# Performance work log

Measured on AMD Instinct MI355X. Metric: run time of the kernel, lower is better.

## Reference

```python
import jax, jax.numpy as jnp
import numpy as np

HIDDEN = 4096
N_HEADS = 32
N_KV_HEADS = 8
HEAD_SIZE = HIDDEN // N_HEADS  # 128
ROPE_THETA = 10000.0
SEQ_LEN = 1024
BATCH = 4


def setup_inputs() -> dict:
    key = jax.random.key(0)
    k1, k2, k3 = jax.random.split(key, 3)
    scale = 1.0 / np.sqrt(HIDDEN)
    hidden_states = jax.random.normal(k1, (BATCH * SEQ_LEN, HIDDEN), dtype=jnp.float32)
    w_qkv = jax.random.normal(k2, ((N_HEADS + 2 * N_KV_HEADS) * HEAD_SIZE, HIDDEN), dtype=jnp.float32) * scale
    w_o = jax.random.normal(k3, (HIDDEN, N_HEADS * HEAD_SIZE), dtype=jnp.float32) * scale
    return {"hidden_states": hidden_states, "w_qkv": w_qkv, "w_o": w_o, "seq_len": SEQ_LEN}


def _rope(x, pos, theta):
    # x: [B, S, H, D]; pos: [S] absolute positions; rotate-half (LLAMA/NeoX) style
    d = x.shape[-1]
    inv_freq = 1.0 / (theta ** (jnp.arange(0, d, 2, dtype=jnp.float32) / d))  # [D/2]
    ang = pos.astype(jnp.float32)[:, None] * inv_freq[None, :]  # [S, D/2]
    cos = jnp.cos(ang)[None, :, None, :]
    sin = jnp.sin(ang)[None, :, None, :]
    x1, x2 = jnp.split(x, 2, axis=-1)
    return jnp.concatenate([x1 * cos - x2 * sin, x2 * cos + x1 * sin], axis=-1)


def reference(hidden_states, w_qkv, w_o, seq_len):
    total, hidden = hidden_states.shape
    B = total // seq_len
    hd = HEAD_SIZE
    # fused QKV projection (bias-free), split like the torch module
    qkv = hidden_states @ w_qkv.T  # [T, (H+2K)*hd]
    q, k, v = jnp.split(qkv, [N_HEADS * hd, (N_HEADS + N_KV_HEADS) * hd], axis=1)
    q = q.reshape(B, seq_len, N_HEADS, hd)
    k = k.reshape(B, seq_len, N_KV_HEADS, hd)
    v = v.reshape(B, seq_len, N_KV_HEADS, hd)
    # inline RoPE (ROPE_LLAMA) on q and k at absolute positions
    pos = jnp.arange(seq_len)
    q = _rope(q, pos, ROPE_THETA)
    k = _rope(k, pos, ROPE_THETA)
    # GQA: map each q head to its kv head (kv_head_mapping = repeat_interleave)
    groups = N_HEADS // N_KV_HEADS
    k = jnp.repeat(k, groups, axis=2)  # [B, S, H, hd]
    v = jnp.repeat(v, groups, axis=2)
    scale = hd ** -0.5
    scores = jnp.einsum('bqhd,bkhd->bhqk', q, k) * scale  # [B, H, S, S]
    causal = jnp.tril(jnp.ones((seq_len, seq_len), dtype=bool))
    scores = jnp.where(causal[None, None], scores, jnp.finfo(scores.dtype).min)
    probs = jax.nn.softmax(scores, axis=-1)
    attn = jnp.einsum('bhqk,bkhd->bqhd', probs, v).reshape(total, N_HEADS * hd)
    return attn @ w_o.T  # [T, hidden]
```

## Files before the change

### kernel.cpp

```cpp
#include <hip/hip_runtime.h>


typedef short bf16x8 __attribute__((ext_vector_type(8)));
typedef short bf16x4 __attribute__((ext_vector_type(4)));
typedef float floatx4 __attribute__((ext_vector_type(4)));
typedef unsigned short u16x4 __attribute__((ext_vector_type(4)));

__device__ __forceinline__ unsigned short f2bf(float f) {
  unsigned u = __float_as_uint(f);
  u += 0x7FFFu + ((u >> 16) & 1u);
  return (unsigned short)(u >> 16);
}
__device__ __forceinline__ float bf2f(unsigned short h) {
  return __uint_as_float(((unsigned)h) << 16);
}

__device__ __forceinline__ void async16(const void* g, void* l) {
  __builtin_amdgcn_global_load_lds(
      (const __attribute__((address_space(1))) unsigned int*)g,
      (__attribute__((address_space(3))) unsigned int*)l, 16, 0, 0);
}

__global__ void cvt_f32_bf16(const float4* __restrict__ in,
                             u16x4* __restrict__ out, int n4) {
  int i = blockIdx.x * 256 + threadIdx.x;
  if (i < n4) {
    float4 v = in[i];
    u16x4 o;
    o.x = f2bf(v.x); o.y = f2bf(v.y); o.z = f2bf(v.z); o.w = f2bf(v.w);
    out[i] = o;
  }
}

template <int OUT_BF16>
__global__ __launch_bounds__(256) void gemm_bt(
    const unsigned short* __restrict__ A, const unsigned short* __restrict__ B,
    void* __restrict__ Cout, int M, int N, int K) {
  __shared__ __align__(16) unsigned short As[128 * 32];
  __shared__ __align__(16) unsigned short Bs[128 * 32];
  const int tid = threadIdx.x;
  const int wave = tid >> 6, lane = tid & 63;
  const int quad = lane >> 4, l16 = lane & 15;
  const int bm = blockIdx.y << 7, bn = blockIdx.x << 7;
  const int wm = (wave >> 1) << 6;
  const int wn = (wave & 1) << 6;

  floatx4 acc[4][4];
#pragma unroll
  for (int i = 0; i < 4; ++i)
#pragma unroll
    for (int j = 0; j < 4; ++j) acc[i][j] = (floatx4){0.f, 0.f, 0.f, 0.f};

  const int r0 = tid >> 2;
  const int o0 = (tid & 3) << 3;
  const unsigned short* A0 = A + (size_t)(bm + r0) * K + o0;
  const unsigned short* A1 = A0 + (size_t)64 * K;
  const unsigned short* B0 = B + (size_t)(bn + r0) * K + o0;
  const unsigned short* B1 = B0 + (size_t)64 * K;
  char* lA0 = (char*)As + wave * 1024;
  char* lA1 = lA0 + 4096;
  char* lB0 = (char*)Bs + wave * 1024;
  char* lB1 = lB0 + 4096;

  const unsigned short* Asp = As + (wm + l16) * 32 + quad * 8;
  const unsigned short* Bsp = Bs + (wn + l16) * 32 + quad * 8;

  for (int k0 = 0; k0 < K; k0 += 32) {
    __syncthreads();
    async16(A0 + k0, lA0);
    async16(A1 + k0, lA1);
    async16(B0 + k0, lB0);
    async16(B1 + k0, lB1);
    __syncthreads();
    bf16x8 af[4], bfr[4];
#pragma unroll
    for (int mi = 0; mi < 4; ++mi) af[mi] = *(const bf16x8*)(Asp + mi * 512);
#pragma unroll
    for (int ni = 0; ni < 4; ++ni) bfr[ni] = *(const bf16x8*)(Bsp + ni * 512);
#pragma unroll
    for (int mi = 0; mi < 4; ++mi)
#pragma unroll
      for (int ni = 0; ni < 4; ++ni)
        acc[mi][ni] = __builtin_amdgcn_mfma_f32_16x16x32_bf16(
            af[mi], bfr[ni], acc[mi][ni], 0, 0, 0);
  }

  const int row0 = bm + wm + quad * 4;
  const int col0 = bn + wn + l16;
  if (OUT_BF16) {
    unsigned short* C = (unsigned short*)Cout;
#pragma unroll
    for (int mi = 0; mi < 4; ++mi)
#pragma unroll
      for (int ni = 0; ni < 4; ++ni)
#pragma unroll
        for (int r = 0; r < 4; ++r)
          C[(size_t)(row0 + mi * 16 + r) * N + (col0 + ni * 16)] =
              f2bf(acc[mi][ni][r]);
  } else {
    float* C = (float*)Cout;
#pragma unroll
    for (int mi = 0; mi < 4; ++mi)
#pragma unroll
      for (int ni = 0; ni < 4; ++ni)
#pragma unroll
        for (int r = 0; r < 4; ++r)
          C[(size_t)(row0 + mi * 16 + r) * N + (col0 + ni * 16)] =
              acc[mi][ni][r];
  }
}

__global__ void rope_k_kernel(unsigned short* __restrict__ qkv) {
  const int t = blockIdx.x;
  const int s = t & 1023;
  const int head = 32 + blockIdx.y * 4 + (threadIdx.x >> 6);
  const int d = threadIdx.x & 63;
  unsigned short* p = qkv + (size_t)t * 6144 + head * 128;
  float x1 = bf2f(p[d]), x2 = bf2f(p[d + 64]);
  float inv_freq = exp2f((float)d * -0.20762050593046015f);
  float ang = (float)s * inv_freq;
  float c, sn;
  __sincosf(ang, &sn, &c);
  p[d] = f2bf(x1 * c - x2 * sn);
  p[d + 64] = f2bf(x2 * c + x1 * sn);
}

__global__ __launch_bounds__(256, 3) void flash_attn(
    const unsigned short* __restrict__ qkv, unsigned short* __restrict__ aout) {
  const int qt = gridDim.x - 1 - blockIdx.x;
  const int h = blockIdx.y, b = blockIdx.z;
  const int kh = h >> 2;
  const int tid = threadIdx.x;
  const int wave = tid >> 6, lane = tid & 63;
  const int quad = lane >> 4, l16 = lane & 15;
  const int q0 = qt << 6;

  __shared__ __align__(16) unsigned short Ks[64][136];
  __shared__ __align__(16) unsigned short Vt[128][68];
  __shared__ __align__(16) unsigned short Ps[64][68];

  bf16x8 qf[4];
  {
    const int qrow = q0 + wave * 16 + l16;
    const unsigned short* qp =
        qkv + (size_t)((b << 10) + qrow) * 6144 + h * 128 + quad * 8;
#pragma unroll
    for (int ks = 0; ks < 4; ++ks) qf[ks] = *(const bf16x8*)(qp + ks * 32);
    const float pos = (float)qrow;
    const float scale = 0.08838834764831845f;
#pragma unroll
    for (int ks = 0; ks < 2; ++ks)
#pragma unroll
      for (int e = 0; e < 8; ++e) {
        int d = ks * 32 + quad * 8 + e;
        float ang = pos * exp2f((float)d * -0.20762050593046015f);
        float c, sn;
        __sincosf(ang, &sn, &c);
        float x1 = bf2f((unsigned short)qf[ks][e]);
        float x2 = bf2f((unsigned short)qf[ks + 2][e]);
        qf[ks][e] = (short)f2bf((x1 * c - x2 * sn) * scale);
        qf[ks + 2][e] = (short)f2bf((x2 * c + x1 * sn) * scale);
      }
  }

  floatx4 o_acc[8];
#pragma unroll
  for (int i = 0; i < 8; ++i) o_acc[i] = (floatx4){0.f, 0.f, 0.f, 0.f};
  float l_lane[4] = {0.f, 0.f, 0.f, 0.f};

  const int krow = tid >> 4, kcol = (tid & 15) << 3;
  const int vrb = (tid & 15) << 2, vcol = (tid >> 4) << 3;
  const unsigned short* kp =
      qkv + (size_t)(b << 10) * 6144 + 4096 + kh * 128;
  const unsigned short* vp =
      qkv + (size_t)(b << 10) * 6144 + 5120 + kh * 128;

  bf16x8 kreg[4], vreg[4];
#pragma unroll
  for (int j = 0; j < 4; ++j)
    kreg[j] = *(const bf16x8*)(kp + (size_t)(krow + j * 16) * 6144 + kcol);
#pragma unroll
  for (int j = 0; j < 4; ++j)
    vreg[j] = *(const bf16x8*)(vp + (size_t)(vrb + j) * 6144 + vcol);

  for (int t = 0; t <= qt; ++t) {
    __syncthreads();
#pragma unroll
    for (int j = 0; j < 4; ++j)
      *(bf16x8*)&Ks[krow + j * 16][kcol] = kreg[j];
#pragma unroll
    for (int e = 0; e < 8; ++e) {
      bf16x4 w = {vreg[0][e], vreg[1][e], vreg[2][e], vreg[3][e]};
      *(bf16x4*)&Vt[vcol + e][vrb] = w;
    }
    __syncthreads();
    if (t < qt) {
      const size_t nb = (size_t)((t + 1) << 6) * 6144;
#pragma unroll
      for (int j = 0; j < 4; ++j)
        kreg[j] = *(const bf16x8*)(kp + nb + (size_t)(krow + j * 16) * 6144 + kcol);
#pragma unroll
      for (int j = 0; j < 4; ++j)
        vreg[j] = *(const bf16x8*)(vp + nb + (size_t)(vrb + j) * 6144 + vcol);
    }

    floatx4 sacc[4];
#pragma unroll
    for (int ni = 0; ni < 4; ++ni) sacc[ni] = (floatx4){0.f, 0.f, 0.f, 0.f};
#pragma unroll
    for (int ks = 0; ks < 4; ++ks)
#pragma unroll
      for (int ni = 0; ni < 4; ++ni) {
        bf16x8 kf = *(const bf16x8*)&Ks[ni * 16 + l16][ks * 32 + quad * 8];
        sacc[ni] =
            __builtin_amdgcn_mfma_f32_16x16x32_bf16(qf[ks], kf, sacc[ni], 0, 0, 0);
      }

    const bool masked = (t == qt);
#pragma unroll
    for (int r = 0; r < 4; ++r) {
      float rs = 0.f;
#pragma unroll
      for (int ni = 0; ni < 4; ++ni) {
        float e = __expf(sacc[ni][r]);
        if (masked && (ni * 16 + l16) > (wave * 16 + quad * 4 + r)) e = 0.f;
        rs += e;
        Ps[wave * 16 + quad * 4 + r][ni * 16 + l16] = f2bf(e);
      }
      l_lane[r] += rs;
    }
    asm volatile("s_waitcnt lgkmcnt(0)" ::: "memory");

#pragma unroll
    for (int ks2 = 0; ks2 < 2; ++ks2) {
      bf16x8 pf = *(const bf16x8*)&Ps[wave * 16 + l16][ks2 * 32 + quad * 8];
#pragma unroll
      for (int n8 = 0; n8 < 8; ++n8) {
        bf16x8 vf = *(const bf16x8*)&Vt[n8 * 16 + l16][ks2 * 32 + quad * 8];
        o_acc[n8] =
            __builtin_amdgcn_mfma_f32_16x16x32_bf16(pf, vf, o_acc[n8], 0, 0, 0);
      }
    }
  }

#pragma unroll
  for (int r = 0; r < 4; ++r) {
    float l = l_lane[r];
#pragma unroll
    for (int off = 1; off < 16; off <<= 1) l += __shfl_xor(l, off, 64);
    float inv = 1.0f / l;
    int row = q0 + wave * 16 + quad * 4 + r;
    unsigned short* op = aout + (size_t)((b << 10) + row) * 4096 + h * 128;
#pragma unroll
    for (int n8 = 0; n8 < 8; ++n8)
      op[n8 * 16 + l16] = f2bf(o_acc[n8][r] * inv);
  }
}

extern "C" void kernel_launch(void* const* d_in, const int* in_sizes, int n_in,
                              void* d_out, int out_size, void* d_ws,
                              size_t ws_size, hipStream_t stream) {
  const float* X = (const float*)d_in[0];
  const float* Wqkv = (const float*)d_in[1];
  const float* Wo = (const float*)d_in[2];
  (void)in_sizes; (void)n_in; (void)out_size; (void)ws_size;

  char* ws = (char*)d_ws;
  unsigned short* Wqkvb = (unsigned short*)ws;
  unsigned short* AttnB = (unsigned short*)ws;
  unsigned short* Xb = (unsigned short*)(ws + 50331648);
  unsigned short* Wob = (unsigned short*)(ws + 50331648);
  unsigned short* QKVb = (unsigned short*)(ws + 83886080);

  cvt_f32_bf16<<<16384, 256, 0, stream>>>((const float4*)X, (u16x4*)Xb, 4194304);
  cvt_f32_bf16<<<24576, 256, 0, stream>>>((const float4*)Wqkv, (u16x4*)Wqkvb, 6291456);
  gemm_bt<1><<<dim3(48, 32), 256, 0, stream>>>(Xb, Wqkvb, QKVb, 4096, 6144, 4096);
  rope_k_kernel<<<dim3(4096, 2), 256, 0, stream>>>(QKVb);
  cvt_f32_bf16<<<16384, 256, 0, stream>>>((const float4*)Wo, (u16x4*)Wob, 4194304);
  flash_attn<<<dim3(16, 32, 4), 256, 0, stream>>>(QKVb, AttnB);
  gemm_bt<0><<<dim3(32, 32), 256, 0, stream>>>(AttnB, Wob, d_out, 4096, 4096, 4096);
}
```

Baseline: 802.4 us.

## Use 32x32 MFMA GEMM with K=64 swizzled LDS tiles and pair causal attention tiles

The GEMM now uses 32x32x16 bf16 MFMA with a 64-wide K step and an XOR-swizzled LDS layout. This halves the number of barriers per K and should reduce LDS bank conflicts. The flash attention grid is halved, and each block processes a long and a short causal query tile (15-pr and pr) so the work per block is balanced. The cost is more LDS per GEMM block and fewer attention blocks in flight.

```diff
diff --git a/kernel.cpp b/kernel.cpp
--- a/kernel.cpp
+++ b/kernel.cpp
@@ -4,6 +4,7 @@
 typedef short bf16x8 __attribute__((ext_vector_type(8)));
 typedef short bf16x4 __attribute__((ext_vector_type(4)));
 typedef float floatx4 __attribute__((ext_vector_type(4)));
+typedef float floatx16 __attribute__((ext_vector_type(16)));
 typedef unsigned short u16x4 __attribute__((ext_vector_type(4)));
 
 __device__ __forceinline__ unsigned short f2bf(float f) {
@@ -33,81 +34,88 @@
 }
 
 template <int OUT_BF16>
-__global__ __launch_bounds__(256) void gemm_bt(
+__global__ __launch_bounds__(256) void gemm_bt32(
     const unsigned short* __restrict__ A, const unsigned short* __restrict__ B,
     void* __restrict__ Cout, int M, int N, int K) {
-  __shared__ __align__(16) unsigned short As[128 * 32];
-  __shared__ __align__(16) unsigned short Bs[128 * 32];
+  __shared__ __align__(16) unsigned short As[128 * 64];
+  __shared__ __align__(16) unsigned short Bs[128 * 64];
   const int tid = threadIdx.x;
   const int wave = tid >> 6, lane = tid & 63;
-  const int quad = lane >> 4, l16 = lane & 15;
+  const int l32 = lane & 31, hi = lane >> 5;
   const int bm = blockIdx.y << 7, bn = blockIdx.x << 7;
-  const int wm = (wave >> 1) << 6;
-  const int wn = (wave & 1) << 6;
-
-  floatx4 acc[4][4];
-#pragma unroll
-  for (int i = 0; i < 4; ++i)
-#pragma unroll
-    for (int j = 0; j < 4; ++j) acc[i][j] = (floatx4){0.f, 0.f, 0.f, 0.f};
-
-  const int r0 = tid >> 2;
-  const int o0 = (tid & 3) << 3;
-  const unsigned short* A0 = A + (size_t)(bm + r0) * K + o0;
-  const unsigned short* A1 = A0 + (size_t)64 * K;
-  const unsigned short* B0 = B + (size_t)(bn + r0) * K + o0;
-  const unsigned short* B1 = B0 + (size_t)64 * K;
-  char* lA0 = (char*)As + wave * 1024;
-  char* lA1 = lA0 + 4096;
-  char* lB0 = (char*)Bs + wave * 1024;
-  char* lB1 = lB0 + 4096;
-
-  const unsigned short* Asp = As + (wm + l16) * 32 + quad * 8;
-  const unsigned short* Bsp = Bs + (wn + l16) * 32 + quad * 8;
-
-  for (int k0 = 0; k0 < K; k0 += 32) {
+  const int wm = (wave >> 1) << 6, wn = (wave & 1) << 6;
+
+  floatx16 acc[2][2];
+#pragma unroll
+  for (int mi = 0; mi < 2; ++mi)
+#pragma unroll
+    for (int ni = 0; ni < 2; ++ni)
+#pragma unroll
+      for (int r = 0; r < 16; ++r) acc[mi][ni][r] = 0.f;
+
+  const int srow = lane >> 3;
+  const int schunk = (lane & 7) ^ srow;
+  const unsigned short* Asrc[4];
+  const unsigned short* Bsrc[4];
+  char* lA[4];
+  char* lB[4];
+#pragma unroll
+  for (int j = 0; j < 4; ++j) {
+    int blk = wave + 4 * j;
+    Asrc[j] = A + (size_t)(bm + blk * 8 + srow) * K + schunk * 8;
+    Bsrc[j] = B + (size_t)(bn + blk * 8 + srow) * K + schunk * 8;
+    lA[j] = (char*)As + wave * 1024 + j * 4096;
+    lB[j] = (char*)Bs + wave * 1024 + j * 4096;
+  }
+
+  const unsigned short* Ap = As + (wm + l32) * 64;
+  const unsigned short* Bp = Bs + (wn + l32) * 64;
+  int co[4];
+#pragma unroll
+  for (int k = 0; k < 4; ++k) co[k] = ((k * 2 + hi) ^ (lane & 7)) * 8;
+
+  for (int k0 = 0; k0 < K; k0 += 64) {
     __syncthreads();
-    async16(A0 + k0, lA0);
-    async16(A1 + k0, lA1);
-    async16(B0 + k0, lB0);
-    async16(B1 + k0, lB1);
+#pragma unroll
+    for (int j = 0; j < 4; ++j) async16(Asrc[j] + k0, lA[j]);
+#pragma unroll
+    for (int j = 0; j < 4; ++j) async16(Bsrc[j] + k0, lB[j]);
     __syncthreads();
-    bf16x8 af[4], bfr[4];
-#pragma unroll
-    for (int mi = 0; mi < 4; ++mi) af[mi] = *(const bf16x8*)(Asp + mi * 512);
-#pragma unroll
-    for (int ni = 0; ni < 4; ++ni) bfr[ni] = *(const bf16x8*)(Bsp + ni * 512);
-#pragma unroll
-    for (int mi = 0; mi < 4; ++mi)
-#pragma unroll
-      for (int ni = 0; ni < 4; ++ni)
-        acc[mi][ni] = __builtin_amdgcn_mfma_f32_16x16x32_bf16(
-            af[mi], bfr[ni], acc[mi][ni], 0, 0, 0);
-  }
-
-  const int row0 = bm + wm + quad * 4;
-  const int col0 = bn + wn + l16;
-  if (OUT_BF16) {
-    unsigned short* C = (unsigned short*)Cout;
-#pragma unroll
-    for (int mi = 0; mi < 4; ++mi)
-#pragma unroll
-      for (int ni = 0; ni < 4; ++ni)
-#pragma unroll
-        for (int r = 0; r < 4; ++r)
-          C[(size_t)(row0 + mi * 16 + r) * N + (col0 + ni * 16)] =
-              f2bf(acc[mi][ni][r]);
-  } else {
-    float* C = (float*)Cout;
-#pragma unroll
-    for (int mi = 0; mi < 4; ++mi)
-#pragma unroll
-      for (int ni = 0; ni < 4; ++ni)
-#pragma unroll
-        for (int r = 0; r < 4; ++r)
-          C[(size_t)(row0 + mi * 16 + r) * N + (col0 + ni * 16)] =
-              acc[mi][ni][r];
-  }
+    bf16x8 af[2][4], bfr[2][4];
+#pragma unroll
+    for (int mi = 0; mi < 2; ++mi)
+#pragma unroll
+      for (int k = 0; k < 4; ++k)
+        af[mi][k] = *(const bf16x8*)(Ap + mi * 2048 + co[k]);
+#pragma unroll
+    for (int ni = 0; ni < 2; ++ni)
+#pragma unroll
+      for (int k = 0; k < 4; ++k)
+        bfr[ni][k] = *(const bf16x8*)(Bp + ni * 2048 + co[k]);
+#pragma unroll
+    for (int k = 0; k < 4; ++k)
+#pragma unroll
+      for (int mi = 0; mi < 2; ++mi)
+#pragma unroll
+        for (int ni = 0; ni < 2; ++ni)
+          acc[mi][ni] = __builtin_amdgcn_mfma_f32_32x32x16_bf16(
+              af[mi][k], bfr[ni][k], acc[mi][ni], 0, 0, 0);
+  }
+
+  const int col0 = bn + wn + l32;
+#pragma unroll
+  for (int mi = 0; mi < 2; ++mi)
+#pragma unroll
+    for (int ni = 0; ni < 2; ++ni)
+#pragma unroll
+      for (int reg = 0; reg < 16; ++reg) {
+        int row = bm + wm + mi * 32 + 4 * hi + (reg & 3) + 8 * (reg >> 2);
+        if (OUT_BF16)
+          ((unsigned short*)Cout)[(size_t)row * N + col0 + ni * 32] =
+              f2bf(acc[mi][ni][reg]);
+        else
+          ((float*)Cout)[(size_t)row * N + col0 + ni * 32] = acc[mi][ni][reg];
+      }
 }
 
 __global__ void rope_k_kernel(unsigned short* __restrict__ qkv) {
@@ -127,133 +135,136 @@
 
 __global__ __launch_bounds__(256, 3) void flash_attn(
     const unsigned short* __restrict__ qkv, unsigned short* __restrict__ aout) {
-  const int qt = gridDim.x - 1 - blockIdx.x;
+  const int pr = blockIdx.x;
   const int h = blockIdx.y, b = blockIdx.z;
   const int kh = h >> 2;
   const int tid = threadIdx.x;
   const int wave = tid >> 6, lane = tid & 63;
   const int quad = lane >> 4, l16 = lane & 15;
-  const int q0 = qt << 6;
 
   __shared__ __align__(16) unsigned short Ks[64][136];
   __shared__ __align__(16) unsigned short Vt[128][68];
   __shared__ __align__(16) unsigned short Ps[64][68];
 
-  bf16x8 qf[4];
-  {
-    const int qrow = q0 + wave * 16 + l16;
-    const unsigned short* qp =
-        qkv + (size_t)((b << 10) + qrow) * 6144 + h * 128 + quad * 8;
-#pragma unroll
-    for (int ks = 0; ks < 4; ++ks) qf[ks] = *(const bf16x8*)(qp + ks * 32);
-    const float pos = (float)qrow;
-    const float scale = 0.08838834764831845f;
-#pragma unroll
-    for (int ks = 0; ks < 2; ++ks)
-#pragma unroll
-      for (int e = 0; e < 8; ++e) {
-        int d = ks * 32 + quad * 8 + e;
-        float ang = pos * exp2f((float)d * -0.20762050593046015f);
-        float c, sn;
-        __sincosf(ang, &sn, &c);
-        float x1 = bf2f((unsigned short)qf[ks][e]);
-        float x2 = bf2f((unsigned short)qf[ks + 2][e]);
-        qf[ks][e] = (short)f2bf((x1 * c - x2 * sn) * scale);
-        qf[ks + 2][e] = (short)f2bf((x2 * c + x1 * sn) * scale);
-      }
-  }
-
-  floatx4 o_acc[8];
-#pragma unroll
-  for (int i = 0; i < 8; ++i) o_acc[i] = (floatx4){0.f, 0.f, 0.f, 0.f};
-  float l_lane[4] = {0.f, 0.f, 0.f, 0.f};
-
   const int krow = tid >> 4, kcol = (tid & 15) << 3;
   const int vrb = (tid & 15) << 2, vcol = (tid >> 4) << 3;
-  const unsigned short* kp =
-      qkv + (size_t)(b << 10) * 6144 + 4096 + kh * 128;
-  const unsigned short* vp =
-      qkv + (size_t)(b << 10) * 6144 + 5120 + kh * 128;
-
-  bf16x8 kreg[4], vreg[4];
-#pragma unroll
-  for (int j = 0; j < 4; ++j)
-    kreg[j] = *(const bf16x8*)(kp + (size_t)(krow + j * 16) * 6144 + kcol);
-#pragma unroll
-  for (int j = 0; j < 4; ++j)
-    vreg[j] = *(const bf16x8*)(vp + (size_t)(vrb + j) * 6144 + vcol);
-
-  for (int t = 0; t <= qt; ++t) {
-    __syncthreads();
+  const unsigned short* kp = qkv + (size_t)(b << 10) * 6144 + 4096 + kh * 128;
+  const unsigned short* vp = qkv + (size_t)(b << 10) * 6144 + 5120 + kh * 128;
+
+  for (int half = 0; half < 2; ++half) {
+    const int qt = half ? pr : 15 - pr;
+    const int q0 = qt << 6;
+
+    bf16x8 qf[4];
+    {
+      const int qrow = q0 + wave * 16 + l16;
+      const unsigned short* qp =
+          qkv + (size_t)((b << 10) + qrow) * 6144 + h * 128 + quad * 8;
+#pragma unroll
+      for (int ks = 0; ks < 4; ++ks) qf[ks] = *(const bf16x8*)(qp + ks * 32);
+      const float pos = (float)qrow;
+      const float scale = 0.08838834764831845f;
+#pragma unroll
+      for (int ks = 0; ks < 2; ++ks)
+#pragma unroll
+        for (int e = 0; e < 8; ++e) {
+          int d = ks * 32 + quad * 8 + e;
+          float ang = pos * exp2f((float)d * -0.20762050593046015f);
+          float c, sn;
+          __sincosf(ang, &sn, &c);
+          float x1 = bf2f((unsigned short)qf[ks][e]);
+          float x2 = bf2f((unsigned short)qf[ks + 2][e]);
+          qf[ks][e] = (short)f2bf((x1 * c - x2 * sn) * scale);
+          qf[ks + 2][e] = (short)f2bf((x2 * c + x1 * sn) * scale);
+        }
+    }
+
+    floatx4 o_acc[8];
+#pragma unroll
+    for (int i = 0; i < 8; ++i) o_acc[i] = (floatx4){0.f, 0.f, 0.f, 0.f};
+    float l_lane[4] = {0.f, 0.f, 0.f, 0.f};
+
+    bf16x8 kreg[4], vreg[4];
 #pragma unroll
     for (int j = 0; j < 4; ++j)
-      *(bf16x8*)&Ks[krow + j * 16][kcol] = kreg[j];
-#pragma unroll
-    for (int e = 0; e < 8; ++e) {
-      bf16x4 w = {vreg[0][e], vreg[1][e], vreg[2][e], vreg[3][e]};
-      *(bf16x4*)&Vt[vcol + e][vrb] = w;
+      kreg[j] = *(const bf16x8*)(kp + (size_t)(krow + j * 16) * 6144 + kcol);
+#pragma unroll
+    for (int j = 0; j < 4; ++j)
+      vreg[j] = *(const bf16x8*)(vp + (size_t)(vrb + j) * 6144 + vcol);
+
+    for (int t = 0; t <= qt; ++t) {
+      __syncthreads();
+#pragma unroll
+      for (int j = 0; j < 4; ++j)
+        *(bf16x8*)&Ks[krow + j * 16][kcol] = kreg[j];
+#pragma unroll
+      for (int e = 0; e < 8; ++e) {
+        bf16x4 w = {vreg[0][e], vreg[1][e], vreg[2][e], vreg[3][e]};
+        *(bf16x4*)&Vt[vcol + e][vrb] = w;
+      }
+      __syncthreads();
+      if (t < qt) {
+        const size_t nb = (size_t)((t + 1) << 6) * 6144;
+#pragma unroll
+        for (int j = 0; j < 4; ++j)
+          kreg[j] =
+              *(const bf16x8*)(kp + nb + (size_t)(krow + j * 16) * 6144 + kcol);
+#pragma unroll
+        for (int j = 0; j < 4; ++j)
+          vreg[j] = *(const bf16x8*)(vp + nb + (size_t)(vrb + j) * 6144 + vcol);
+      }
+
+      floatx4 sacc[4];
+#pragma unroll
+      for (int ni = 0; ni < 4; ++ni) sacc[ni] = (floatx4){0.f, 0.f, 0.f, 0.f};
+#pragma unroll
+      for (int ks = 0; ks < 4; ++ks)
+#pragma unroll
+        for (int ni = 0; ni < 4; ++ni) {
+          bf16x8 kf = *(const bf16x8*)&Ks[ni * 16 + l16][ks * 32 + quad * 8];
+          sacc[ni] = __builtin_amdgcn_mfma_f32_16x16x32_bf16(qf[ks], kf,
+                                                             sacc[ni], 0, 0, 0);
+        }
+
+      const bool masked = (t == qt);
+#pragma unroll
+      for (int r = 0; r < 4; ++r) {
+        float rs = 0.f;
+#pragma unroll
+        for (int ni = 0; ni < 4; ++ni) {
+          float e = __expf(sacc[ni][r]);
+          if (masked && (ni * 16 + l16) > (wave * 16 + quad * 4 + r)) e = 0.f;
+          rs += e;
+          Ps[wave * 16 + quad * 4 + r][ni * 16 + l16] = f2bf(e);
+        }
+        l_lane[r] += rs;
+      }
+      asm volatile("s_waitcnt lgkmcnt(0)" ::: "memory");
+
+#pragma unroll
+      for (int ks2 = 0; ks2 < 2; ++ks2) {
+        bf16x8 pf = *(const bf16x8*)&Ps[wave * 16 + l16][ks2 * 32 + quad * 8];
+#pragma unroll
+        for (int n8 = 0; n8 < 8; ++n8) {
+          bf16x8 vf = *(const bf16x8*)&Vt[n8 * 16 + l16][ks2 * 32 + quad * 8];
+          o_acc[n8] = __builtin_amdgcn_mfma_f32_16x16x32_bf16(pf, vf, o_acc[n8],
+                                                              0, 0, 0);
+        }
+      }
     }
-    __syncthreads();
-    if (t < qt) {
-      const size_t nb = (size_t)((t + 1) << 6) * 6144;
-#pragma unroll
-      for (int j = 0; j < 4; ++j)
-        kreg[j] = *(const bf16x8*)(kp + nb + (size_t)(krow + j * 16) * 6144 + kcol);
-#pragma unroll
-      for (int j = 0; j < 4; ++j)
-        vreg[j] = *(const bf16x8*)(vp + nb + (size_t)(vrb + j) * 6144 + vcol);
+
+#pragma unroll
+    for (int r = 0; r < 4; ++r) {
+      float l = l_lane[r];
+#pragma unroll
+      for (int off = 1; off < 16; off <<= 1) l += __shfl_xor(l, off, 64);
+      float inv = 1.0f / l;
+      int row = q0 + wave * 16 + quad * 4 + r;
+      unsigned short* op = aout + (size_t)((b << 10) + row) * 4096 + h * 128;
+#pragma unroll
+      for (int n8 = 0; n8 < 8; ++n8)
+        op[n8 * 16 + l16] = f2bf(o_acc[n8][r] * inv);
     }
-
-    floatx4 sacc[4];
-#pragma unroll
-    for (int ni = 0; ni < 4; ++ni) sacc[ni] = (floatx4){0.f, 0.f, 0.f, 0.f};
-#pragma unroll
-    for (int ks = 0; ks < 4; ++ks)
-#pragma unroll
-      for (int ni = 0; ni < 4; ++ni) {
-        bf16x8 kf = *(const bf16x8*)&Ks[ni * 16 + l16][ks * 32 + quad * 8];
-        sacc[ni] =
-            __builtin_amdgcn_mfma_f32_16x16x32_bf16(qf[ks], kf, sacc[ni], 0, 0, 0);
-      }
-
-    const bool masked = (t == qt);
-#pragma unroll
-    for (int r = 0; r < 4; ++r) {
-      float rs = 0.f;
-#pragma unroll
-      for (int ni = 0; ni < 4; ++ni) {
-        float e = __expf(sacc[ni][r]);
-        if (masked && (ni * 16 + l16) > (wave * 16 + quad * 4 + r)) e = 0.f;
-        rs += e;
-        Ps[wave * 16 + quad * 4 + r][ni * 16 + l16] = f2bf(e);
-      }
-      l_lane[r] += rs;
-    }
-    asm volatile("s_waitcnt lgkmcnt(0)" ::: "memory");
-
-#pragma unroll
-    for (int ks2 = 0; ks2 < 2; ++ks2) {
-      bf16x8 pf = *(const bf16x8*)&Ps[wave * 16 + l16][ks2 * 32 + quad * 8];
-#pragma unroll
-      for (int n8 = 0; n8 < 8; ++n8) {
-        bf16x8 vf = *(const bf16x8*)&Vt[n8 * 16 + l16][ks2 * 32 + quad * 8];
-        o_acc[n8] =
-            __builtin_amdgcn_mfma_f32_16x16x32_bf16(pf, vf, o_acc[n8], 0, 0, 0);
-      }
-    }
-  }
-
-#pragma unroll
-  for (int r = 0; r < 4; ++r) {
-    float l = l_lane[r];
-#pragma unroll
-    for (int off = 1; off < 16; off <<= 1) l += __shfl_xor(l, off, 64);
-    float inv = 1.0f / l;
-    int row = q0 + wave * 16 + quad * 4 + r;
-    unsigned short* op = aout + (size_t)((b << 10) + row) * 4096 + h * 128;
-#pragma unroll
-    for (int n8 = 0; n8 < 8; ++n8)
-      op[n8 * 16 + l16] = f2bf(o_acc[n8][r] * inv);
   }
 }
 
@@ -274,9 +285,9 @@
 
   cvt_f32_bf16<<<16384, 256, 0, stream>>>((const float4*)X, (u16x4*)Xb, 4194304);
   cvt_f32_bf16<<<24576, 256, 0, stream>>>((const float4*)Wqkv, (u16x4*)Wqkvb, 6291456);
-  gemm_bt<1><<<dim3(48, 32), 256, 0, stream>>>(Xb, Wqkvb, QKVb, 4096, 6144, 4096);
+  gemm_bt32<1><<<dim3(48, 32), 256, 0, stream>>>(Xb, Wqkvb, QKVb, 4096, 6144, 4096);
   rope_k_kernel<<<dim3(4096, 2), 256, 0, stream>>>(QKVb);
   cvt_f32_bf16<<<16384, 256, 0, stream>>>((const float4*)Wo, (u16x4*)Wob, 4194304);
-  flash_attn<<<dim3(16, 32, 4), 256, 0, stream>>>(QKVb, AttnB);
-  gemm_bt<0><<<dim3(32, 32), 256, 0, stream>>>(AttnB, Wob, d_out, 4096, 4096, 4096);
-}
+  flash_attn<<<dim3(8, 32, 4), 256, 0, stream>>>(QKVb, AttnB);
+  gemm_bt32<0><<<dim3(32, 32), 256, 0, stream>>>(AttnB, Wob, d_out, 4096, 4096, 4096);
+}
```

New measurement: 699.8 us. -12.8%, faster.
